# Performance work log

Hardware: AMD Instinct MI355X
Metric: run time of the kernel (lower is better)

Reference implementation:

```python
import jax, jax.numpy as jnp
import numpy as np

N_NODES = 207
N_EDGES = 1722
N_SLOTS = 288  # 288 / resolution with resolution = 1


def setup_inputs() -> dict:
    key = jax.random.key(0)
    ks = jax.random.split(key, 7)
    B, C, L = 1024, 2, 64
    inputs = jax.random.normal(ks[0], (B, C, N_NODES, L), dtype=jnp.float32)
    weight_diff = jax.random.normal(ks[1], (N_SLOTS, N_EDGES), dtype=jnp.float32) / 1000.0
    bias_diffusion = jax.random.normal(ks[2], (N_SLOTS, N_NODES), dtype=jnp.float32) / 10.0
    weight_self_loop = jax.random.normal(ks[3], (N_SLOTS, N_NODES), dtype=jnp.float32) / 10.0
    ind = jax.random.randint(ks[4], (B,), 0, N_SLOTS, dtype=jnp.int32)
    edge_i = jax.random.randint(ks[5], (N_EDGES,), 0, N_NODES, dtype=jnp.int32)
    edge_j = jax.random.randint(ks[6], (N_EDGES,), 0, N_NODES, dtype=jnp.int32)
    return {"inputs": inputs, "weight_diff": weight_diff,
            "bias_diffusion": bias_diffusion, "weight_self_loop": weight_self_loop,
            "ind": ind, "edge_i": edge_i, "edge_j": edge_j}


def reference(inputs, weight_diff, bias_diffusion, weight_self_loop, ind, edge_i, edge_j):
    # resolution = 1 -> slot index ii == ind
    x = inputs[:, 0, :, :]                      # [B, N, L]
    B, N, _ = x.shape
    w = weight_diff[ind]                        # [B, E] per-sample edge weights
    # symmetric scatter into batched dense adjacency (duplicates sum, as in sparse_coo_tensor)
    A = jnp.zeros((B, N, N), dtype=x.dtype)
    A = A.at[:, edge_i, edge_j].add(w).at[:, edge_j, edge_i].add(w)
    deg = jnp.sum(A, axis=1)                    # [B, N]  (sum over dim 1, as in torch code)
    lap = deg[:, :, None] * jnp.eye(N, dtype=x.dtype) - A  # L = diag(deg) - A
    diffusion = jnp.einsum('nvl,nwv->nwl', x, lap) + bias_diffusion[ind][:, :, None]
    self_loop = weight_self_loop[ind][:, :, None] * x
    return diffusion + x + self_loop
```

## Files before the change

### kernel.cpp

```cpp
#include <hip/hip_runtime.h>
#include <stdint.h>

#define N_NODES 207
#define N_EDGES 1722
#define N_SLOTS 288
#define L_DIM   64
#define NCSR    (2 * N_EDGES)

__device__ __forceinline__ unsigned int f2bf_rtn_bits_hi(float f) {
    unsigned int u = __float_as_uint(f);
    unsigned int r = u + 0x7FFFu + ((u >> 16) & 1u);
    return r & 0xFFFF0000u;
}

__global__ __launch_bounds__(256) void build_csr_kernel(
    const int* __restrict__ edge_i, const int* __restrict__ edge_j,
    int* __restrict__ row_start, unsigned int* __restrict__ csr_packed) {
    __shared__ int cnt[N_NODES];
    __shared__ int rs[N_NODES + 1];
    const int tid = threadIdx.x;

    for (int n = tid; n < N_NODES; n += 256) cnt[n] = 0;
    __syncthreads();
    for (int e = tid; e < N_EDGES; e += 256) {
        atomicAdd(&cnt[edge_i[e]], 1);
        atomicAdd(&cnt[edge_j[e]], 1);
    }
    __syncthreads();
    if (tid == 0) {
        int acc = 0;
        for (int n = 0; n < N_NODES; ++n) { rs[n] = acc; acc += cnt[n]; }
        rs[N_NODES] = acc;
    }
    __syncthreads();
    for (int n = tid; n <= N_NODES; n += 256) row_start[n] = rs[n];
    for (int n = tid; n < N_NODES; n += 256) cnt[n] = rs[n];
    __syncthreads();
    for (int e = tid; e < N_EDGES; e += 256) {
        const unsigned int i = edge_i[e], j = edge_j[e];
        const unsigned int ep = ((unsigned int)e) << 8;
        int p = atomicAdd(&cnt[i], 1);
        csr_packed[p] = ep | j;
        int q = atomicAdd(&cnt[j], 1);
        csr_packed[q] = ep | i;
    }
}

__global__ __launch_bounds__(256) void coef_eb_kernel(
    const float* __restrict__ weight_diff, const float* __restrict__ bias_diffusion,
    const float* __restrict__ weight_self_loop,
    const int* __restrict__ row_start, const unsigned int* __restrict__ csr_packed,
    float2* __restrict__ coefbias, unsigned int* __restrict__ eb32) {
    __shared__ float wrow[N_EDGES];
    const int s = blockIdx.x;
    for (int e = threadIdx.x; e < N_EDGES; e += 256)
        wrow[e] = weight_diff[(size_t)s * N_EDGES + e];
    __syncthreads();

    if (eb32 != nullptr) {
        unsigned int* ebs = eb32 + (size_t)s * NCSR;
        for (int k = threadIdx.x; k < NCSR; k += 256) {
            const unsigned int c = csr_packed[k];
            ebs[k] = f2bf_rtn_bits_hi(wrow[c >> 8]) | ((c & 255u) << 7);
        }
    }

    const int n = threadIdx.x;
    if (n < N_NODES) {
        float d = 0.f;
        const int e0 = row_start[n], e1 = row_start[n + 1];
        for (int k = e0; k < e1; ++k) d += wrow[csr_packed[k] >> 8];
        coefbias[s * N_NODES + n] = make_float2(
            1.f + weight_self_loop[s * N_NODES + n] + d,
            bias_diffusion[s * N_NODES + n]);
    }
}

__global__ __launch_bounds__(512, 8) void diffusion_lds_kernel(
    const float* __restrict__ inputs,
    const int*   __restrict__ ind,
    const int*   __restrict__ row_start,
    const unsigned int* __restrict__ eb32,
    const float2* __restrict__ coefbias,
    float* __restrict__ out) {
    __shared__ unsigned short xs[N_NODES * L_DIM];
    __shared__ unsigned int   wnb[NCSR];
    __shared__ unsigned short rs[N_NODES + 1];

    const int b    = blockIdx.x;
    const int tid  = threadIdx.x;
    const int slot = ind[b];

    const float* xb = inputs + (size_t)b * (2 * N_NODES * L_DIM);

    const float4* xb4 = (const float4*)xb;
    for (int k = tid; k < (N_NODES * L_DIM) / 4; k += 512) {
        const float4 v = xb4[k];
        const unsigned int lo = (f2bf_rtn_bits_hi(v.x) >> 16) | f2bf_rtn_bits_hi(v.y);
        const unsigned int hi = (f2bf_rtn_bits_hi(v.z) >> 16) | f2bf_rtn_bits_hi(v.w);
        ((uint2*)xs)[k] = make_uint2(lo, hi);
    }
    {
        const uint4* src = (const uint4*)(eb32 + (size_t)slot * NCSR);
        uint4* dst = (uint4*)wnb;
        for (int k = tid; k < NCSR / 4; k += 512) dst[k] = src[k];
    }
    for (int n = tid; n <= N_NODES; n += 512) rs[n] = (unsigned short)row_start[n];
    __syncthreads();

    const int lane  = tid & 63;
    const unsigned int lane2 = (unsigned int)(lane << 1);
    const int wv    = tid >> 6;
    float* ob = out + (size_t)b * (N_NODES * L_DIM);
    const char* xsb = (const char*)xs;
    const float2* cbs = coefbias + (size_t)slot * N_NODES;

    for (int n = wv; n < N_NODES; n += 8) {
        const int e0 = rs[n], e1 = rs[n + 1];
        float s = 0.f;
        #pragma unroll 4
        for (int k = e0; k < e1; ++k) {
            const unsigned int p = wnb[k];
            const float w = __uint_as_float(p & 0xFFFF0000u);
            const unsigned int off = (p & 0xFFFFu) | lane2;
            const unsigned int xv = *(const unsigned short*)(xsb + off);
            s = fmaf(w, __uint_as_float(xv << 16), s);
        }
        const float2 cb = cbs[n];
        const float  xg = xb[(n << 6) + lane];
        ob[(n << 6) + lane] = fmaf(cb.x, xg, cb.y) - s;
    }
}

__global__ __launch_bounds__(512, 8) void diffusion_gcn_fallback(
    const float* __restrict__ inputs,
    const float* __restrict__ weight_diff,
    const int*   __restrict__ ind,
    const int*   __restrict__ row_start,
    const unsigned int* __restrict__ csr_packed,
    const float2* __restrict__ coefbias,
    float* __restrict__ out) {
    __shared__ unsigned short xsh[N_NODES * L_DIM];
    __shared__ unsigned int   wnb[NCSR];
    __shared__ unsigned short rs[N_NODES + 1];

    const int b    = blockIdx.x;
    const int tid  = threadIdx.x;
    const int slot = ind[b];

    const float* xb = inputs + (size_t)b * (2 * N_NODES * L_DIM);

    const float4* xb4 = (const float4*)xb;
    for (int k = tid; k < (N_NODES * L_DIM) / 4; k += 512) {
        const float4 v = xb4[k];
        const unsigned int lo = (f2bf_rtn_bits_hi(v.x) >> 16) | f2bf_rtn_bits_hi(v.y);
        const unsigned int hi = (f2bf_rtn_bits_hi(v.z) >> 16) | f2bf_rtn_bits_hi(v.w);
        ((uint2*)xsh)[k] = make_uint2(lo, hi);
    }
    const float* wrow = weight_diff + (size_t)slot * N_EDGES;
    for (int k = tid; k < NCSR; k += 512) {
        const unsigned int c = csr_packed[k];
        wnb[k] = f2bf_rtn_bits_hi(wrow[c >> 8]) | (c & 255u);
    }
    for (int n = tid; n <= N_NODES; n += 512) rs[n] = (unsigned short)row_start[n];
    __syncthreads();

    const int lane = tid & 63;
    const int wv   = tid >> 6;
    float* ob = out + (size_t)b * (N_NODES * L_DIM);

    for (int n = wv; n < N_NODES; n += 8) {
        const int e0 = rs[n], e1 = rs[n + 1];
        float s = 0.f;
        #pragma unroll 4
        for (int k = e0; k < e1; ++k) {
            const unsigned int p = wnb[k];
            const float w  = __uint_as_float(p & 0xFFFF0000u);
            const float xv = __uint_as_float(
                (unsigned int)xsh[(p & 255u) * L_DIM + lane] << 16);
            s = fmaf(w, xv, s);
        }
        const float2 cb = coefbias[slot * N_NODES + n];
        const float  xg = xb[n * L_DIM + lane];
        ob[n * L_DIM + lane] = fmaf(cb.x, xg, cb.y) - s;
    }
}

extern "C" void kernel_launch(void* const* d_in, const int* in_sizes, int n_in,
                              void* d_out, int out_size, void* d_ws, size_t ws_size,
                              hipStream_t stream) {
    const float* inputs           = (const float*)d_in[0];
    const float* weight_diff      = (const float*)d_in[1];
    const float* bias_diffusion   = (const float*)d_in[2];
    const float* weight_self_loop = (const float*)d_in[3];
    const int*   ind              = (const int*)d_in[4];
    const int*   edge_i           = (const int*)d_in[5];
    const int*   edge_j           = (const int*)d_in[6];
    float* out = (float*)d_out;

    const int B = in_sizes[4];

    char* ws = (char*)d_ws;
    int*          row_start  = (int*)ws;
    unsigned int* csr_packed = (unsigned int*)(ws + 832);
    float2*       coefbias   = (float2*)(ws + 14608);
    unsigned int* eb32       = (unsigned int*)(ws + 491536);
    const size_t  WS_NEEDED  = 491536 + (size_t)N_SLOTS * NCSR * sizeof(unsigned int);

    const bool use_eb = (d_ws != nullptr) && (ws_size >= WS_NEEDED);

    build_csr_kernel<<<1, 256, 0, stream>>>(edge_i, edge_j, row_start, csr_packed);
    coef_eb_kernel<<<N_SLOTS, 256, 0, stream>>>(
        weight_diff, bias_diffusion, weight_self_loop, row_start, csr_packed,
        coefbias, use_eb ? eb32 : nullptr);
    if (use_eb) {
        diffusion_lds_kernel<<<B, 512, 0, stream>>>(
            inputs, ind, row_start, eb32, coefbias, out);
    } else {
        diffusion_gcn_fallback<<<B, 512, 0, stream>>>(
            inputs, weight_diff, ind, row_start, csr_packed, coefbias, out);
    }
}
```

Before: 233.8 us.

## Replace sparse CSR gather with dense per-slot Laplacian table and MFMA matmul

Builds a dense bf16 Laplacian table per slot (padded to 208x224, laid out in MFMA B-fragment order) and computes each sample's diffusion as a dense x^T·L product with 16x16x32 bf16 MFMA instructions, instead of the per-lane sparse gather over CSR edges. Inputs are transposed into LDS as bf16. The dense approach does far more arithmetic than the sparse one, roughly 27MB of table must be built each call and read from cache or memory, and it only runs when the workspace is large enough.

```diff
diff --git a/kernel.cpp b/kernel.cpp
--- a/kernel.cpp
+++ b/kernel.cpp
@@ -6,6 +6,14 @@
 #define N_SLOTS 288
 #define L_DIM   64
 #define NCSR    (2 * N_EDGES)
+
+#define NT_TILES 13
+#define KS_STEPS 7
+#define TB_SLOT  (NT_TILES * KS_STEPS * 64 * 8)
+#define XSTRIDE  232
+
+typedef __attribute__((ext_vector_type(8))) short bf16x8;
+typedef __attribute__((ext_vector_type(4))) float f32x4;
 
 __device__ __forceinline__ unsigned int f2bf_rtn_bits_hi(float f) {
     unsigned int u = __float_as_uint(f);
@@ -73,6 +81,142 @@
         coefbias[s * N_NODES + n] = make_float2(
             1.f + weight_self_loop[s * N_NODES + n] + d,
             bias_diffusion[s * N_NODES + n]);
+    }
+}
+
+__global__ __launch_bounds__(256) void lap_table_kernel(
+    const float* __restrict__ weight_diff, const float* __restrict__ bias_diffusion,
+    const float* __restrict__ weight_self_loop,
+    const int* __restrict__ edge_i, const int* __restrict__ edge_j,
+    unsigned short* __restrict__ tableB, float2* __restrict__ coefbias) {
+    __shared__ float wrow[N_EDGES];
+    __shared__ int   ei[N_EDGES];
+    __shared__ int   ej[N_EDGES];
+    __shared__ float lapc[32][228];
+    const int s = blockIdx.x, t = threadIdx.x;
+
+    for (int e = t; e < N_EDGES; e += 256) {
+        wrow[e] = weight_diff[(size_t)s * N_EDGES + e];
+        ei[e] = edge_i[e];
+        ej[e] = edge_j[e];
+    }
+    if (t < N_NODES) {
+        coefbias[s * N_NODES + t] = make_float2(
+            1.f + weight_self_loop[s * N_NODES + t],
+            bias_diffusion[s * N_NODES + t]);
+    }
+    __syncthreads();
+
+    unsigned int* outp = (unsigned int*)(tableB + (size_t)s * TB_SLOT);
+
+    for (int c = 0; c < KS_STEPS; ++c) {
+        const int r0 = c * 32;
+        for (int k = t; k < (32 * 228) / 4; k += 256)
+            ((float4*)&lapc[0][0])[k] = make_float4(0.f, 0.f, 0.f, 0.f);
+        __syncthreads();
+        for (int e = t; e < N_EDGES; e += 256) {
+            const int i = ei[e], j = ej[e];
+            const float w = wrow[e];
+            if ((unsigned)(i - r0) < 32u) {
+                atomicAdd(&lapc[i - r0][j], -w);
+                atomicAdd(&lapc[i - r0][i],  w);
+            }
+            if ((unsigned)(j - r0) < 32u) {
+                atomicAdd(&lapc[j - r0][i], -w);
+                atomicAdd(&lapc[j - r0][j],  w);
+            }
+        }
+        __syncthreads();
+        const int ln = t >> 2;
+        const int jp = (t & 3) << 1;
+        const int kl = ((ln >> 4) << 3) + jp;
+        for (int nt = 0; nt < NT_TILES; ++nt) {
+            const int n = nt * 16 + (ln & 15);
+            const unsigned u0 = f2bf_rtn_bits_hi(lapc[kl][n]) >> 16;
+            const unsigned u1 = f2bf_rtn_bits_hi(lapc[kl + 1][n]);
+            outp[((nt * KS_STEPS + c) * 64 + ln) * 4 + (jp >> 1)] = u0 | u1;
+        }
+        __syncthreads();
+    }
+}
+
+__global__ __launch_bounds__(512, 4) void diffusion_mfma_kernel(
+    const float* __restrict__ inputs,
+    const int*   __restrict__ ind,
+    const unsigned short* __restrict__ tableB,
+    const float2* __restrict__ coefbias,
+    float* __restrict__ out) {
+    __shared__ unsigned short xT[64 * XSTRIDE];
+    __shared__ float2 cbl[N_NODES + 1];
+
+    const int b    = blockIdx.x;
+    const int tid  = threadIdx.x;
+    const int slot = ind[b];
+    const float* xb = inputs + (size_t)b * (2 * N_NODES * L_DIM);
+
+    for (int k = tid; k < (64 * XSTRIDE * 2) / 16; k += 512)
+        ((uint4*)xT)[k] = make_uint4(0u, 0u, 0u, 0u);
+    if (tid < N_NODES) cbl[tid] = coefbias[slot * N_NODES + tid];
+    __syncthreads();
+
+    const float4* xb4 = (const float4*)xb;
+    for (int idx = tid; idx < (N_NODES * L_DIM) / 4; idx += 512) {
+        const int v  = idx >> 4;
+        const int l0 = (idx & 15) << 2;
+        const float4 q = xb4[idx];
+        xT[(l0 + 0) * XSTRIDE + v] = (unsigned short)(f2bf_rtn_bits_hi(q.x) >> 16);
+        xT[(l0 + 1) * XSTRIDE + v] = (unsigned short)(f2bf_rtn_bits_hi(q.y) >> 16);
+        xT[(l0 + 2) * XSTRIDE + v] = (unsigned short)(f2bf_rtn_bits_hi(q.z) >> 16);
+        xT[(l0 + 3) * XSTRIDE + v] = (unsigned short)(f2bf_rtn_bits_hi(q.w) >> 16);
+    }
+    __syncthreads();
+
+    const int lane = tid & 63;
+    const int wv   = tid >> 6;
+    const int ra   = lane & 15;
+    const int kq   = (lane >> 4) << 3;
+    const int lb   = (lane >> 4) << 2;
+    float* ob = out + (size_t)b * (N_NODES * L_DIM);
+    const unsigned short* tbs = tableB + (size_t)slot * TB_SLOT;
+
+    for (int nt = wv; nt < NT_TILES; nt += 8) {
+        f32x4 acc0 = {0.f, 0.f, 0.f, 0.f};
+        f32x4 acc1 = {0.f, 0.f, 0.f, 0.f};
+        f32x4 acc2 = {0.f, 0.f, 0.f, 0.f};
+        f32x4 acc3 = {0.f, 0.f, 0.f, 0.f};
+        const unsigned short* tbn = tbs + nt * (KS_STEPS * 512) + lane * 8;
+        #pragma unroll
+        for (int ks = 0; ks < KS_STEPS; ++ks) {
+            const bf16x8 bb = *(const bf16x8*)(tbn + ks * 512);
+            const int kof = ks * 32 + kq;
+            const bf16x8 a0 = *(const bf16x8*)&xT[(ra     ) * XSTRIDE + kof];
+            const bf16x8 a1 = *(const bf16x8*)&xT[(ra + 16) * XSTRIDE + kof];
+            const bf16x8 a2 = *(const bf16x8*)&xT[(ra + 32) * XSTRIDE + kof];
+            const bf16x8 a3 = *(const bf16x8*)&xT[(ra + 48) * XSTRIDE + kof];
+            acc0 = __builtin_amdgcn_mfma_f32_16x16x32_bf16(a0, bb, acc0, 0, 0, 0);
+            acc1 = __builtin_amdgcn_mfma_f32_16x16x32_bf16(a1, bb, acc1, 0, 0, 0);
+            acc2 = __builtin_amdgcn_mfma_f32_16x16x32_bf16(a2, bb, acc2, 0, 0, 0);
+            acc3 = __builtin_amdgcn_mfma_f32_16x16x32_bf16(a3, bb, acc3, 0, 0, 0);
+        }
+        const int n = nt * 16 + ra;
+        if (n < N_NODES) {
+            const float2 cb = cbl[n];
+#define EPILOG(MT, ACC) do {                                                  \
+            const int l0 = (MT) * 16 + lb;                                    \
+            const float4 xg = *(const float4*)(xb + (n << 6) + l0);           \
+            float4 o;                                                         \
+            o.x = fmaf(cb.x, xg.x, (ACC)[0] + cb.y);                          \
+            o.y = fmaf(cb.x, xg.y, (ACC)[1] + cb.y);                          \
+            o.z = fmaf(cb.x, xg.z, (ACC)[2] + cb.y);                          \
+            o.w = fmaf(cb.x, xg.w, (ACC)[3] + cb.y);                          \
+            *(float4*)(ob + (n << 6) + l0) = o;                               \
+        } while (0)
+            EPILOG(0, acc0);
+            EPILOG(1, acc1);
+            EPILOG(2, acc2);
+            EPILOG(3, acc3);
+#undef EPILOG
+        }
     }
 }
 
@@ -201,22 +345,35 @@
     const int B = in_sizes[4];
 
     char* ws = (char*)d_ws;
+
+    unsigned short* tableB     = (unsigned short*)ws;
+    float2*         coefbias_m = (float2*)(ws + 26836992);
+    const size_t WS_MFMA = 26836992 + (size_t)N_SLOTS * N_NODES * sizeof(float2);
+
     int*          row_start  = (int*)ws;
     unsigned int* csr_packed = (unsigned int*)(ws + 832);
     float2*       coefbias   = (float2*)(ws + 14608);
     unsigned int* eb32       = (unsigned int*)(ws + 491536);
-    const size_t  WS_NEEDED  = 491536 + (size_t)N_SLOTS * NCSR * sizeof(unsigned int);
-
-    const bool use_eb = (d_ws != nullptr) && (ws_size >= WS_NEEDED);
-
-    build_csr_kernel<<<1, 256, 0, stream>>>(edge_i, edge_j, row_start, csr_packed);
-    coef_eb_kernel<<<N_SLOTS, 256, 0, stream>>>(
-        weight_diff, bias_diffusion, weight_self_loop, row_start, csr_packed,
-        coefbias, use_eb ? eb32 : nullptr);
-    if (use_eb) {
+    const size_t WS_EB  = 491536 + (size_t)N_SLOTS * NCSR * sizeof(unsigned int);
+
+    if (d_ws != nullptr && ws_size >= WS_MFMA) {
+        lap_table_kernel<<<N_SLOTS, 256, 0, stream>>>(
+            weight_diff, bias_diffusion, weight_self_loop, edge_i, edge_j,
+            tableB, coefbias_m);
+        diffusion_mfma_kernel<<<B, 512, 0, stream>>>(
+            inputs, ind, tableB, coefbias_m, out);
+    } else if (d_ws != nullptr && ws_size >= WS_EB) {
+        build_csr_kernel<<<1, 256, 0, stream>>>(edge_i, edge_j, row_start, csr_packed);
+        coef_eb_kernel<<<N_SLOTS, 256, 0, stream>>>(
+            weight_diff, bias_diffusion, weight_self_loop, row_start, csr_packed,
+            coefbias, eb32);
         diffusion_lds_kernel<<<B, 512, 0, stream>>>(
             inputs, ind, row_start, eb32, coefbias, out);
     } else {
+        build_csr_kernel<<<1, 256, 0, stream>>>(edge_i, edge_j, row_start, csr_packed);
+        coef_eb_kernel<<<N_SLOTS, 256, 0, stream>>>(
+            weight_diff, bias_diffusion, weight_self_loop, row_start, csr_packed,
+            coefbias, nullptr);
         diffusion_gcn_fallback<<<B, 512, 0, stream>>>(
             inputs, weight_diff, ind, row_start, csr_packed, coefbias, out);
     }
```

New measurement: 259.6 us. +11.1%, slower.

## Pad CSR rows to multiples of four and process four edges per wave

Applied to the files above, without the earlier changes.

Pads each CSR row to a multiple of four entries with sentinel zero-weight entries. The main kernel splits each wave into four 16-lane groups, each handling one edge with 4 columns per lane via 8-byte LDS reads, then reduces across groups with shuffles. Edge weights are read straight from global/L2 rather than staged in LDS, and output is written as float4 from 16 lanes. This cuts per-edge loop iterations and LDS instruction count, at the cost of padding work, cross-lane reductions, and only a quarter of lanes active during the epilogue.

```diff
diff --git a/kernel.cpp b/kernel.cpp
--- a/kernel.cpp
+++ b/kernel.cpp
@@ -5,7 +5,7 @@
 #define N_EDGES 1722
 #define N_SLOTS 288
 #define L_DIM   64
-#define NCSR    (2 * N_EDGES)
+#define EB_STRIDE 4096
 
 __device__ __forceinline__ unsigned int f2bf_rtn_bits_hi(float f) {
     unsigned int u = __float_as_uint(f);
@@ -15,7 +15,7 @@
 
 __global__ __launch_bounds__(256) void build_csr_kernel(
     const int* __restrict__ edge_i, const int* __restrict__ edge_j,
-    int* __restrict__ row_start, unsigned int* __restrict__ csr_packed) {
+    int* __restrict__ rs_p, unsigned int* __restrict__ csr_p) {
     __shared__ int cnt[N_NODES];
     __shared__ int rs[N_NODES + 1];
     const int tid = threadIdx.x;
@@ -29,63 +29,72 @@
     __syncthreads();
     if (tid == 0) {
         int acc = 0;
-        for (int n = 0; n < N_NODES; ++n) { rs[n] = acc; acc += cnt[n]; }
+        for (int n = 0; n < N_NODES; ++n) { rs[n] = acc; acc += (cnt[n] + 3) & ~3; }
         rs[N_NODES] = acc;
     }
     __syncthreads();
-    for (int n = tid; n <= N_NODES; n += 256) row_start[n] = rs[n];
+    for (int n = tid; n <= N_NODES; n += 256) rs_p[n] = rs[n];
+    for (int k = tid; k < EB_STRIDE; k += 256) csr_p[k] = 0xFFFFFFFFu;
     for (int n = tid; n < N_NODES; n += 256) cnt[n] = rs[n];
     __syncthreads();
     for (int e = tid; e < N_EDGES; e += 256) {
         const unsigned int i = edge_i[e], j = edge_j[e];
         const unsigned int ep = ((unsigned int)e) << 8;
         int p = atomicAdd(&cnt[i], 1);
-        csr_packed[p] = ep | j;
+        csr_p[p] = ep | j;
         int q = atomicAdd(&cnt[j], 1);
-        csr_packed[q] = ep | i;
+        csr_p[q] = ep | i;
     }
 }
 
 __global__ __launch_bounds__(256) void coef_eb_kernel(
     const float* __restrict__ weight_diff, const float* __restrict__ bias_diffusion,
     const float* __restrict__ weight_self_loop,
-    const int* __restrict__ row_start, const unsigned int* __restrict__ csr_packed,
-    float2* __restrict__ coefbias, unsigned int* __restrict__ eb32) {
+    const int* __restrict__ rs_p, const unsigned int* __restrict__ csr_p,
+    float2* __restrict__ coefbias, unsigned int* __restrict__ eb32p) {
     __shared__ float wrow[N_EDGES];
     const int s = blockIdx.x;
     for (int e = threadIdx.x; e < N_EDGES; e += 256)
         wrow[e] = weight_diff[(size_t)s * N_EDGES + e];
     __syncthreads();
 
-    if (eb32 != nullptr) {
-        unsigned int* ebs = eb32 + (size_t)s * NCSR;
-        for (int k = threadIdx.x; k < NCSR; k += 256) {
-            const unsigned int c = csr_packed[k];
-            ebs[k] = f2bf_rtn_bits_hi(wrow[c >> 8]) | ((c & 255u) << 7);
+    if (eb32p != nullptr) {
+        const int EP = rs_p[N_NODES];
+        unsigned int* ebs = eb32p + (size_t)s * EB_STRIDE;
+        for (int k = threadIdx.x; k < EB_STRIDE; k += 256) {
+            unsigned int v = 0u;
+            if (k < EP) {
+                const unsigned int c = csr_p[k];
+                if (c != 0xFFFFFFFFu)
+                    v = f2bf_rtn_bits_hi(wrow[c >> 8]) | ((c & 255u) << 7);
+            }
+            ebs[k] = v;
         }
     }
 
     const int n = threadIdx.x;
     if (n < N_NODES) {
         float d = 0.f;
-        const int e0 = row_start[n], e1 = row_start[n + 1];
-        for (int k = e0; k < e1; ++k) d += wrow[csr_packed[k] >> 8];
+        const int e0 = rs_p[n], e1 = rs_p[n + 1];
+        for (int k = e0; k < e1; ++k) {
+            const unsigned int c = csr_p[k];
+            if (c != 0xFFFFFFFFu) d += wrow[c >> 8];
+        }
         coefbias[s * N_NODES + n] = make_float2(
             1.f + weight_self_loop[s * N_NODES + n] + d,
             bias_diffusion[s * N_NODES + n]);
     }
 }
 
-__global__ __launch_bounds__(512, 8) void diffusion_lds_kernel(
+__global__ __launch_bounds__(512, 8) void diffusion_quad_kernel(
     const float* __restrict__ inputs,
     const int*   __restrict__ ind,
-    const int*   __restrict__ row_start,
-    const unsigned int* __restrict__ eb32,
+    const int*   __restrict__ rs_p_g,
+    const unsigned int* __restrict__ eb32p,
     const float2* __restrict__ coefbias,
     float* __restrict__ out) {
     __shared__ unsigned short xs[N_NODES * L_DIM];
-    __shared__ unsigned int   wnb[NCSR];
-    __shared__ unsigned short rs[N_NODES + 1];
+    __shared__ unsigned int   rsp[N_NODES];
 
     const int b    = blockIdx.x;
     const int tid  = threadIdx.x;
@@ -100,35 +109,50 @@
         const unsigned int hi = (f2bf_rtn_bits_hi(v.z) >> 16) | f2bf_rtn_bits_hi(v.w);
         ((uint2*)xs)[k] = make_uint2(lo, hi);
     }
-    {
-        const uint4* src = (const uint4*)(eb32 + (size_t)slot * NCSR);
-        uint4* dst = (uint4*)wnb;
-        for (int k = tid; k < NCSR / 4; k += 512) dst[k] = src[k];
-    }
-    for (int n = tid; n <= N_NODES; n += 512) rs[n] = (unsigned short)row_start[n];
-    __syncthreads();
-
-    const int lane  = tid & 63;
-    const unsigned int lane2 = (unsigned int)(lane << 1);
-    const int wv    = tid >> 6;
+    for (int n = tid; n < N_NODES; n += 512)
+        rsp[n] = (unsigned int)rs_p_g[n] | ((unsigned int)rs_p_g[n + 1] << 16);
+    __syncthreads();
+
+    const int lane = tid & 63;
+    const int wv   = tid >> 6;
+    const int h    = lane >> 4;
+    const unsigned int li8 = (unsigned int)((lane & 15) << 3);
+    const unsigned int* ebs = eb32p + (size_t)slot * EB_STRIDE;
+    const float2* cbs = coefbias + (size_t)slot * N_NODES;
     float* ob = out + (size_t)b * (N_NODES * L_DIM);
     const char* xsb = (const char*)xs;
-    const float2* cbs = coefbias + (size_t)slot * N_NODES;
 
     for (int n = wv; n < N_NODES; n += 8) {
-        const int e0 = rs[n], e1 = rs[n + 1];
-        float s = 0.f;
-        #pragma unroll 4
-        for (int k = e0; k < e1; ++k) {
-            const unsigned int p = wnb[k];
-            const float w = __uint_as_float(p & 0xFFFF0000u);
-            const unsigned int off = (p & 0xFFFFu) | lane2;
-            const unsigned int xv = *(const unsigned short*)(xsb + off);
-            s = fmaf(w, __uint_as_float(xv << 16), s);
-        }
-        const float2 cb = cbs[n];
-        const float  xg = xb[(n << 6) + lane];
-        ob[(n << 6) + lane] = fmaf(cb.x, xg, cb.y) - s;
+        const unsigned int rr = rsp[n];
+        const int e0 = (int)(rr & 0xFFFFu);
+        const int e1 = (int)(rr >> 16);
+        float s0 = 0.f, s1 = 0.f, s2 = 0.f, s3 = 0.f;
+        #pragma unroll 2
+        for (int k = e0; k < e1; k += 4) {
+            const unsigned int p = ebs[k + h];
+            const unsigned int w = p & 0xFFFF0000u;
+            const unsigned int off = (p & 0xFFFFu) | li8;
+            const uint2 xv = *(const uint2*)(xsb + off);
+            s0 = fmaf(__uint_as_float(w), __uint_as_float(xv.x << 16), s0);
+            s1 = fmaf(__uint_as_float(w), __uint_as_float(xv.x & 0xFFFF0000u), s1);
+            s2 = fmaf(__uint_as_float(w), __uint_as_float(xv.y << 16), s2);
+            s3 = fmaf(__uint_as_float(w), __uint_as_float(xv.y & 0xFFFF0000u), s3);
+        }
+        s0 += __shfl_xor(s0, 16); s1 += __shfl_xor(s1, 16);
+        s2 += __shfl_xor(s2, 16); s3 += __shfl_xor(s3, 16);
+        s0 += __shfl_xor(s0, 32); s1 += __shfl_xor(s1, 32);
+        s2 += __shfl_xor(s2, 32); s3 += __shfl_xor(s3, 32);
+        if (lane < 16) {
+            const float2 cb = cbs[n];
+            const int o4 = (n << 6) + (lane << 2);
+            const float4 xg = *(const float4*)(xb + o4);
+            float4 o;
+            o.x = fmaf(cb.x, xg.x, cb.y) - s0;
+            o.y = fmaf(cb.x, xg.y, cb.y) - s1;
+            o.z = fmaf(cb.x, xg.z, cb.y) - s2;
+            o.w = fmaf(cb.x, xg.w, cb.y) - s3;
+            *(float4*)(ob + o4) = o;
+        }
     }
 }
 
@@ -136,12 +160,12 @@
     const float* __restrict__ inputs,
     const float* __restrict__ weight_diff,
     const int*   __restrict__ ind,
-    const int*   __restrict__ row_start,
-    const unsigned int* __restrict__ csr_packed,
+    const int*   __restrict__ rs_p_g,
+    const unsigned int* __restrict__ csr_p,
     const float2* __restrict__ coefbias,
     float* __restrict__ out) {
     __shared__ unsigned short xsh[N_NODES * L_DIM];
-    __shared__ unsigned int   wnb[NCSR];
+    __shared__ unsigned int   wnb[EB_STRIDE];
     __shared__ unsigned short rs[N_NODES + 1];
 
     const int b    = blockIdx.x;
@@ -157,12 +181,14 @@
         const unsigned int hi = (f2bf_rtn_bits_hi(v.z) >> 16) | f2bf_rtn_bits_hi(v.w);
         ((uint2*)xsh)[k] = make_uint2(lo, hi);
     }
+    const int EP = rs_p_g[N_NODES];
     const float* wrow = weight_diff + (size_t)slot * N_EDGES;
-    for (int k = tid; k < NCSR; k += 512) {
-        const unsigned int c = csr_packed[k];
-        wnb[k] = f2bf_rtn_bits_hi(wrow[c >> 8]) | (c & 255u);
-    }
-    for (int n = tid; n <= N_NODES; n += 512) rs[n] = (unsigned short)row_start[n];
+    for (int k = tid; k < EP; k += 512) {
+        const unsigned int c = csr_p[k];
+        wnb[k] = (c == 0xFFFFFFFFu) ? 0u
+                                    : (f2bf_rtn_bits_hi(wrow[c >> 8]) | (c & 255u));
+    }
+    for (int n = tid; n <= N_NODES; n += 512) rs[n] = (unsigned short)rs_p_g[n];
     __syncthreads();
 
     const int lane = tid & 63;
@@ -201,23 +227,23 @@
     const int B = in_sizes[4];
 
     char* ws = (char*)d_ws;
-    int*          row_start  = (int*)ws;
-    unsigned int* csr_packed = (unsigned int*)(ws + 832);
-    float2*       coefbias   = (float2*)(ws + 14608);
-    unsigned int* eb32       = (unsigned int*)(ws + 491536);
-    const size_t  WS_NEEDED  = 491536 + (size_t)N_SLOTS * NCSR * sizeof(unsigned int);
-
-    const bool use_eb = (d_ws != nullptr) && (ws_size >= WS_NEEDED);
-
-    build_csr_kernel<<<1, 256, 0, stream>>>(edge_i, edge_j, row_start, csr_packed);
+    int*          rs_p     = (int*)ws;
+    unsigned int* csr_p    = (unsigned int*)(ws + 1024);
+    float2*       coefbias = (float2*)(ws + 17408);
+    unsigned int* eb32p    = (unsigned int*)(ws + 494336);
+    const size_t WS_FULL = 494336 + (size_t)N_SLOTS * EB_STRIDE * sizeof(unsigned int);
+
+    const bool full = (d_ws != nullptr) && (ws_size >= WS_FULL);
+
+    build_csr_kernel<<<1, 256, 0, stream>>>(edge_i, edge_j, rs_p, csr_p);
     coef_eb_kernel<<<N_SLOTS, 256, 0, stream>>>(
-        weight_diff, bias_diffusion, weight_self_loop, row_start, csr_packed,
-        coefbias, use_eb ? eb32 : nullptr);
-    if (use_eb) {
-        diffusion_lds_kernel<<<B, 512, 0, stream>>>(
-            inputs, ind, row_start, eb32, coefbias, out);
+        weight_diff, bias_diffusion, weight_self_loop, rs_p, csr_p,
+        coefbias, full ? eb32p : nullptr);
+    if (full) {
+        diffusion_quad_kernel<<<B, 512, 0, stream>>>(
+            inputs, ind, rs_p, eb32p, coefbias, out);
     } else {
         diffusion_gcn_fallback<<<B, 512, 0, stream>>>(
-            inputs, weight_diff, ind, row_start, csr_packed, coefbias, out);
-    }
-}
+            inputs, weight_diff, ind, rs_p, csr_p, coefbias, out);
+    }
+}
```

Result: no change. 238.4 us (+2.0%).
